# Kernel tuning notes

Measured on AMD Instinct MI355X. Metric: run time of the kernel, lower is better.

Reference implementation:

```python
import jax, jax.numpy as jnp
import numpy as np

B, T, D = 16, 4096, 512
N_SLOTS = 64


def setup_inputs() -> dict:
    key = jax.random.key(0)
    ks = jax.random.split(key, 7)
    s = 1.0 / np.sqrt(D)  # keep tanh out of deep saturation, like orthogonal*0.9 init
    return {
        "x_seq": jax.random.normal(ks[0], (B, T, D), jnp.float32),
        "h_tape": jax.random.normal(ks[1], (B, N_SLOTS, D), jnp.float32) * 0.1,
        "h_work": jax.random.normal(ks[2], (B, D), jnp.float32) * 0.1,
        "W_h": jax.random.normal(ks[3], (D, D), jnp.float32) * s,
        "W_x": jax.random.normal(ks[4], (D, D), jnp.float32) * s,
        "b_h": jnp.zeros((D,), jnp.float32),
        "W_write": jax.random.normal(ks[5], (D, D), jnp.float32) * s,
    }


def reference(x_seq, h_tape, h_work, W_h, W_x, b_h, W_write):
    """Dual-memory Elman recurrence.

    Per step t:
      read_t  = softmax(h_tape @ h_work / sqrt(D)) @ h_tape   (content-based tape read)
      h_work  = tanh(W_h h_work + W_x x_t + read_t + b_h)
      tape write: slot (t mod n_slots) <- W_write h_work      (FIFO tape write)
    Returns (h_work_out [B,T,D], h_tape_final [B,S,D], last h_work [B,D]).
    """
    scale = jnp.asarray(1.0 / np.sqrt(D), x_seq.dtype)

    def step(carry, inp):
        tape, h = carry
        x_t, t = inp
        scores = jnp.einsum("bsd,bd->bs", tape, h) * scale        # [B,S]
        attn = jax.nn.softmax(scores, axis=-1)
        read = jnp.einsum("bs,bsd->bd", attn, tape)               # [B,D]
        h_new = jnp.tanh(h @ W_h.T + x_t @ W_x.T + read + b_h)    # [B,D]
        w_vec = h_new @ W_write.T                                 # [B,D]
        slot = t % N_SLOTS
        tape = jax.lax.dynamic_update_slice(tape, w_vec[:, None, :], (0, slot, 0))
        return (tape, h_new), h_new

    xs = (jnp.swapaxes(x_seq, 0, 1), jnp.arange(x_seq.shape[1]))
    (tape_f, _), h_seq = jax.lax.scan(step, (h_tape, h_work), xs)
    h_work_out = jnp.swapaxes(h_seq, 0, 1)  # [B,T,D]
    return h_work_out, tape_f, h_work_out[:, -1]
```

## Files before the change

### kernel.cpp

```cpp
#include <hip/hip_runtime.h>
#include <cstddef>

#define B_SZ   16
#define T_SZ   4096
#define D_SZ   512
#define NSLOT  64
#define NW     16
#define RPW    32
#define TP     36
#define SCALE  0.044194173824159216f

__device__ __align__(8) unsigned long long g_ps2[B_SZ * NW * NSLOT];
__device__ __align__(8) unsigned long long g_hx2[B_SZ * D_SZ];

#define AL(p)    __hip_atomic_load((p),  __ATOMIC_RELAXED, __HIP_MEMORY_SCOPE_AGENT)
#define AS(p,v)  __hip_atomic_store((p), (v), __ATOMIC_RELAXED, __HIP_MEMORY_SCOPE_AGENT)

__device__ __forceinline__ unsigned long long pk(float v, unsigned tag) {
    return ((unsigned long long)tag << 32) | (unsigned long long)__float_as_uint(v);
}

__global__ __launch_bounds__(256)
void xw_gemm_kernel(const float* __restrict__ X, const float* __restrict__ Wx,
                    const float* __restrict__ bh, float* __restrict__ out)
{
    __shared__ float As[16][68];
    __shared__ float Bs[16][68];
    const int m0 = blockIdx.x * 64;
    const int n0 = blockIdx.y * 64;
    const int tid = threadIdx.x;
    const int tr = tid >> 4, tc = tid & 15;
    const int lrow = tid >> 2;
    const int lkk  = (tid & 3) * 4;

    float acc[4][4] = {};

    for (int k0 = 0; k0 < D_SZ; k0 += 16) {
        float4 av = *(const float4*)(X  + (size_t)(m0 + lrow) * D_SZ + k0 + lkk);
        float4 bv = *(const float4*)(Wx + (size_t)(n0 + lrow) * D_SZ + k0 + lkk);
        As[lkk+0][lrow] = av.x; As[lkk+1][lrow] = av.y;
        As[lkk+2][lrow] = av.z; As[lkk+3][lrow] = av.w;
        Bs[lkk+0][lrow] = bv.x; Bs[lkk+1][lrow] = bv.y;
        Bs[lkk+2][lrow] = bv.z; Bs[lkk+3][lrow] = bv.w;
        __syncthreads();
        #pragma unroll
        for (int kk = 0; kk < 16; ++kk) {
            float a[4], b[4];
            #pragma unroll
            for (int i = 0; i < 4; ++i) a[i] = As[kk][tr*4+i];
            #pragma unroll
            for (int j = 0; j < 4; ++j) b[j] = Bs[kk][tc*4+j];
            #pragma unroll
            for (int i = 0; i < 4; ++i)
                #pragma unroll
                for (int j = 0; j < 4; ++j)
                    acc[i][j] = fmaf(a[i], b[j], acc[i][j]);
        }
        __syncthreads();
    }
    #pragma unroll
    for (int i = 0; i < 4; ++i) {
        const int m = m0 + tr*4 + i;
        const int n = n0 + tc*4;
        float4 o;
        o.x = acc[i][0] + bh[n+0];
        o.y = acc[i][1] + bh[n+1];
        o.z = acc[i][2] + bh[n+2];
        o.w = acc[i][3] + bh[n+3];
        *(float4*)(out + (size_t)m * D_SZ + n) = o;
    }
}

__global__ __launch_bounds__(256, 1)
void recurrence_mw(const float* __restrict__ tape0, const float* __restrict__ h0,
                   const float* __restrict__ W_h, const float* __restrict__ W_w,
                   float* __restrict__ out)
{
    __shared__ float tp[NSLOT][TP];
    __shared__ float hh[D_SZ];
    __shared__ float ps_l[NSLOT];
    __shared__ float attn[NSLOT];
    __shared__ float zmv[RPW];
    __shared__ float rp8[8][RPW];

    const int blk = blockIdx.x;
    const int xcd = blk & 7;
    const int jj0 = blk >> 3;
    const int b   = xcd * 2 + (jj0 & 1);
    const int w   = jj0 >> 1;
    const int R0  = w * RPW;
    const int tid = threadIdx.x;
    const int fb  = b * NW;
    const int g16 = tid >> 4, sj = tid & 15;

    if (tid < NSLOT) AS(&g_ps2[(size_t)(fb + w) * NSLOT + tid], 0ULL);
    if (tid < RPW)   AS(&g_hx2[(size_t)b * D_SZ + R0 + tid], 0ULL);

    float4 wh0[8], wh1[8], ww0[8], ww1[8];
    {
        const float* a0 = W_h + (size_t)(R0 + g16)      * D_SZ + 4 * sj;
        const float* a1 = W_h + (size_t)(R0 + g16 + 16) * D_SZ + 4 * sj;
        const float* b0 = W_w + (size_t)(R0 + g16)      * D_SZ + 4 * sj;
        const float* b1 = W_w + (size_t)(R0 + g16 + 16) * D_SZ + 4 * sj;
        #pragma unroll
        for (int i = 0; i < 8; ++i) {
            wh0[i] = *(const float4*)(a0 + 64 * i);
            wh1[i] = *(const float4*)(a1 + 64 * i);
            ww0[i] = *(const float4*)(b0 + 64 * i);
            ww1[i] = *(const float4*)(b1 + 64 * i);
        }
    }

    for (int i = tid; i < NSLOT * RPW; i += 256) {
        const int s = i >> 5, jc = i & 31;
        tp[s][jc] = tape0[((size_t)b * NSLOT + s) * D_SZ + R0 + jc];
    }
    for (int i = tid; i < D_SZ; i += 256) hh[i] = h0[(size_t)b * D_SZ + i];
    __syncthreads();

    float* outb = out + (size_t)b * T_SZ * D_SZ;

    const int sA = tid >> 2, qA = tid & 3;
    const int jB = tid & 31, sg = tid >> 5;

    for (int t = 0; t < T_SZ; ++t) {
        const unsigned tg = (unsigned)(t + 1);
        float xwv = 0.f;
        if (tid < RPW) xwv = outb[(size_t)t * D_SZ + R0 + tid];

        {
            float4 t0 = *(const float4*)&tp[sA][qA * 8];
            float4 t1 = *(const float4*)&tp[sA][qA * 8 + 4];
            float4 ha = *(const float4*)&hh[R0 + qA * 8];
            float4 hb = *(const float4*)&hh[R0 + qA * 8 + 4];
            float acc = t0.x*ha.x + t0.y*ha.y + t0.z*ha.z + t0.w*ha.w
                      + t1.x*hb.x + t1.y*hb.y + t1.z*hb.z + t1.w*hb.w;
            acc += __shfl_xor(acc, 1);
            acc += __shfl_xor(acc, 2);
            if (qA == 0) ps_l[sA] = acc;
        }
        __syncthreads();

        if (tid < NSLOT)
            AS(&g_ps2[(size_t)(fb + w) * NSLOT + tid], pk(ps_l[tid], tg));

        {
            float a0 = 0.f, a1 = 0.f;
            #pragma unroll
            for (int i = 0; i < 8; ++i) {
                float4 hr = *(const float4*)&hh[4 * sj + 64 * i];
                a0 = fmaf(wh0[i].x, hr.x, a0);
                a0 = fmaf(wh0[i].y, hr.y, a0);
                a0 = fmaf(wh0[i].z, hr.z, a0);
                a0 = fmaf(wh0[i].w, hr.w, a0);
                a1 = fmaf(wh1[i].x, hr.x, a1);
                a1 = fmaf(wh1[i].y, hr.y, a1);
                a1 = fmaf(wh1[i].z, hr.z, a1);
                a1 = fmaf(wh1[i].w, hr.w, a1);
            }
            a0 += __shfl_xor(a0, 1); a1 += __shfl_xor(a1, 1);
            a0 += __shfl_xor(a0, 2); a1 += __shfl_xor(a1, 2);
            a0 += __shfl_xor(a0, 4); a1 += __shfl_xor(a1, 4);
            a0 += __shfl_xor(a0, 8); a1 += __shfl_xor(a1, 8);
            if (sj == 0) { zmv[g16] = a0; zmv[g16 + 16] = a1; }
        }

        {
            const unsigned long long* pp = &g_ps2[(size_t)(fb + qA * 4) * NSLOT + sA];
            unsigned long long v0, v1, v2, v3;
            for (;;) {
                v0 = AL(pp + 0 * NSLOT); v1 = AL(pp + 1 * NSLOT);
                v2 = AL(pp + 2 * NSLOT); v3 = AL(pp + 3 * NSLOT);
                if ((unsigned)(v0 >> 32) == tg && (unsigned)(v1 >> 32) == tg &&
                    (unsigned)(v2 >> 32) == tg && (unsigned)(v3 >> 32) == tg) break;
                __builtin_amdgcn_s_sleep(1);
            }
            float acc = __uint_as_float((unsigned)v0) + __uint_as_float((unsigned)v1)
                      + __uint_as_float((unsigned)v2) + __uint_as_float((unsigned)v3);
            acc += __shfl_xor(acc, 1);
            acc += __shfl_xor(acc, 2);
            if (qA == 0) ps_l[sA] = acc * SCALE;
        }
        __syncthreads();

        if (tid < 64) {
            const float v = ps_l[tid];
            float m = v;
            #pragma unroll
            for (int o = 32; o; o >>= 1) m = fmaxf(m, __shfl_xor(m, o));
            const float e = __expf(v - m);
            float s = e;
            #pragma unroll
            for (int o = 32; o; o >>= 1) s += __shfl_xor(s, o);
            attn[tid] = e / s;
        }
        __syncthreads();

        {
            float acc = 0.f;
            #pragma unroll
            for (int s8 = 0; s8 < 8; ++s8)
                acc = fmaf(attn[sg * 8 + s8], tp[sg * 8 + s8][jB], acc);
            rp8[sg][jB] = acc;
        }
        __syncthreads();

        if (tid < RPW) {
            const float rr = rp8[0][tid] + rp8[1][tid] + rp8[2][tid] + rp8[3][tid]
                           + rp8[4][tid] + rp8[5][tid] + rp8[6][tid] + rp8[7][tid];
            const float v = tanhf(zmv[tid] + rr + xwv);
            outb[(size_t)t * D_SZ + R0 + tid] = v;
            AS(&g_hx2[(size_t)b * D_SZ + R0 + tid], pk(v, tg));
        }

        {
            const int d0 = tid * 2;
            const unsigned long long* hp = &g_hx2[(size_t)b * D_SZ + d0];
            unsigned long long v0, v1;
            for (;;) {
                v0 = AL(hp); v1 = AL(hp + 1);
                if ((unsigned)(v0 >> 32) == tg && (unsigned)(v1 >> 32) == tg) break;
                __builtin_amdgcn_s_sleep(1);
            }
            hh[d0]     = __uint_as_float((unsigned)v0);
            hh[d0 + 1] = __uint_as_float((unsigned)v1);
        }
        __syncthreads();

        {
            const int slot = t & (NSLOT - 1);
            float a0 = 0.f, a1 = 0.f;
            #pragma unroll
            for (int i = 0; i < 8; ++i) {
                float4 hr = *(const float4*)&hh[4 * sj + 64 * i];
                a0 = fmaf(ww0[i].x, hr.x, a0);
                a0 = fmaf(ww0[i].y, hr.y, a0);
                a0 = fmaf(ww0[i].z, hr.z, a0);
                a0 = fmaf(ww0[i].w, hr.w, a0);
                a1 = fmaf(ww1[i].x, hr.x, a1);
                a1 = fmaf(ww1[i].y, hr.y, a1);
                a1 = fmaf(ww1[i].z, hr.z, a1);
                a1 = fmaf(ww1[i].w, hr.w, a1);
            }
            a0 += __shfl_xor(a0, 1); a1 += __shfl_xor(a1, 1);
            a0 += __shfl_xor(a0, 2); a1 += __shfl_xor(a1, 2);
            a0 += __shfl_xor(a0, 4); a1 += __shfl_xor(a1, 4);
            a0 += __shfl_xor(a0, 8); a1 += __shfl_xor(a1, 8);
            if (sj == 0) {
                tp[slot][g16]      = a0;
                tp[slot][g16 + 16] = a1;
            }
        }
        __syncthreads();
    }

    float* tout = out + (size_t)B_SZ * T_SZ * D_SZ + (size_t)b * NSLOT * D_SZ;
    for (int i = tid; i < NSLOT * RPW; i += 256) {
        const int s = i >> 5, jc = i & 31;
        tout[(size_t)s * D_SZ + R0 + jc] = tp[s][jc];
    }
    if (tid < RPW) {
        float* lout = out + (size_t)B_SZ * T_SZ * D_SZ
                          + (size_t)B_SZ * NSLOT * D_SZ + (size_t)b * D_SZ;
        lout[R0 + tid] = hh[R0 + tid];
    }
}

extern "C" void kernel_launch(void* const* d_in, const int* in_sizes, int n_in,
                              void* d_out, int out_size, void* d_ws, size_t ws_size,
                              hipStream_t stream)
{
    const float* x_seq   = (const float*)d_in[0];
    const float* h_tape  = (const float*)d_in[1];
    const float* h_work  = (const float*)d_in[2];
    const float* W_h     = (const float*)d_in[3];
    const float* W_x     = (const float*)d_in[4];
    const float* b_h     = (const float*)d_in[5];
    const float* W_write = (const float*)d_in[6];
    float* out = (float*)d_out;

    dim3 g1(T_SZ * B_SZ / 64, D_SZ / 64);
    xw_gemm_kernel<<<g1, 256, 0, stream>>>(x_seq, W_x, b_h, out);

    recurrence_mw<<<B_SZ * NW, 256, 0, stream>>>(h_tape, h_work, W_h, W_write, out);
}
```

Baseline: 15.92 ms.

## Defer tape write to next step and merge per-step grid syncs into one

The per-step schedule is restructured. Each step now does a single combined spin-wait for the partial attention scores and the new h, where before there were two separate cross-block waits. The W_write matvec is folded into the same pass as the W_h matvec on the next step. The newly written slot's score is handled by a small extra exchange (g_q) and a softmax correction, which takes the write off the critical path between h publication and the next step's scores. In exchange it adds a per-step wait on the single-slot dot product, extra softmax bookkeeping, and a final-step flush, which raises correctness risk.

```diff
diff --git a/kernel.cpp b/kernel.cpp
--- a/kernel.cpp
+++ b/kernel.cpp
@@ -10,14 +10,18 @@
 #define TP     36
 #define SCALE  0.044194173824159216f
 
-__device__ __align__(8) unsigned long long g_ps2[B_SZ * NW * NSLOT];
-__device__ __align__(8) unsigned long long g_hx2[B_SZ * D_SZ];
+__device__ __align__(8) unsigned long long g_pb[B_SZ * NW * NSLOT];
+__device__ __align__(8) unsigned long long g_hb[B_SZ * D_SZ];
+__device__ __align__(8) unsigned long long g_q [B_SZ * NW];
 
 #define AL(p)    __hip_atomic_load((p),  __ATOMIC_RELAXED, __HIP_MEMORY_SCOPE_AGENT)
 #define AS(p,v)  __hip_atomic_store((p), (v), __ATOMIC_RELAXED, __HIP_MEMORY_SCOPE_AGENT)
 
 __device__ __forceinline__ unsigned long long pk(float v, unsigned tag) {
     return ((unsigned long long)tag << 32) | (unsigned long long)__float_as_uint(v);
+}
+__device__ __forceinline__ float lo(unsigned long long v) {
+    return __uint_as_float((unsigned)v);
 }
 
 __global__ __launch_bounds__(256)
@@ -76,12 +80,14 @@
                    const float* __restrict__ W_h, const float* __restrict__ W_w,
                    float* __restrict__ out)
 {
-    __shared__ float tp[NSLOT][TP];
-    __shared__ float hh[D_SZ];
-    __shared__ float ps_l[NSLOT];
-    __shared__ float attn[NSLOT];
+    __shared__ __align__(16) float tp[NSLOT][TP];
+    __shared__ __align__(16) float hh[D_SZ];
+    __shared__ __align__(16) float hno[RPW];
+    __shared__ float scr[NSLOT];
+    __shared__ float es[NSLOT];
     __shared__ float zmv[RPW];
     __shared__ float rp8[8][RPW];
+    __shared__ float sml[2];
 
     const int blk = blockIdx.x;
     const int xcd = blk & 7;
@@ -92,9 +98,12 @@
     const int tid = threadIdx.x;
     const int fb  = b * NW;
     const int g16 = tid >> 4, sj = tid & 15;
-
-    if (tid < NSLOT) AS(&g_ps2[(size_t)(fb + w) * NSLOT + tid], 0ULL);
-    if (tid < RPW)   AS(&g_hx2[(size_t)b * D_SZ + R0 + tid], 0ULL);
+    const int sA  = tid >> 2, qA = tid & 3;
+    const int sg  = tid >> 5, jB = tid & 31;
+
+    if (tid < NSLOT) AS(&g_pb[((size_t)fb + w) * NSLOT + tid], 0ULL);
+    if (tid < RPW)   AS(&g_hb[(size_t)b * D_SZ + R0 + tid], 0ULL);
+    if (tid == 0)    AS(&g_q[fb + w], 0ULL);
 
     float4 wh0[8], wh1[8], ww0[8], ww1[8];
     {
@@ -112,79 +121,88 @@
     }
 
     for (int i = tid; i < NSLOT * RPW; i += 256) {
-        const int s = i >> 5, jc = i & 31;
-        tp[s][jc] = tape0[((size_t)b * NSLOT + s) * D_SZ + R0 + jc];
+        const int s = i >> 5, j = i & 31;
+        tp[s][j] = tape0[((size_t)b * NSLOT + s) * D_SZ + R0 + j];
     }
     for (int i = tid; i < D_SZ; i += 256) hh[i] = h0[(size_t)b * D_SZ + i];
     __syncthreads();
 
     float* outb = out + (size_t)b * T_SZ * D_SZ;
 
-    const int sA = tid >> 2, qA = tid & 3;
-    const int jB = tid & 31, sg = tid >> 5;
+    if (tid < RPW) {
+        hno[tid] = hh[R0 + tid];
+        AS(&g_hb[(size_t)b * D_SZ + R0 + tid], pk(hh[R0 + tid], 1u));
+    }
+    __syncthreads();
+    {
+        const float* trow = &tp[sA][8 * qA];
+        float4 t0 = *(const float4*)trow;
+        float4 t1 = *(const float4*)(trow + 4);
+        float4 h0v = *(const float4*)&hno[8 * qA];
+        float4 h1v = *(const float4*)&hno[8 * qA + 4];
+        float pp = t0.x*h0v.x + t0.y*h0v.y + t0.z*h0v.z + t0.w*h0v.w
+                 + t1.x*h1v.x + t1.y*h1v.y + t1.z*h1v.z + t1.w*h1v.w;
+        pp += __shfl_xor(pp, 1);
+        pp += __shfl_xor(pp, 2);
+        if (qA == 0) AS(&g_pb[((size_t)fb + w) * NSLOT + sA], pk(pp, 1u));
+    }
 
     for (int t = 0; t < T_SZ; ++t) {
-        const unsigned tg = (unsigned)(t + 1);
+        const unsigned tgB = (unsigned)(t + 1);
+        const int sp = (t - 1) & 63;
+
         float xwv = 0.f;
         if (tid < RPW) xwv = outb[(size_t)t * D_SZ + R0 + tid];
-
         {
-            float4 t0 = *(const float4*)&tp[sA][qA * 8];
-            float4 t1 = *(const float4*)&tp[sA][qA * 8 + 4];
-            float4 ha = *(const float4*)&hh[R0 + qA * 8];
-            float4 hb = *(const float4*)&hh[R0 + qA * 8 + 4];
-            float acc = t0.x*ha.x + t0.y*ha.y + t0.z*ha.z + t0.w*ha.w
-                      + t1.x*hb.x + t1.y*hb.y + t1.z*hb.z + t1.w*hb.w;
-            acc += __shfl_xor(acc, 1);
-            acc += __shfl_xor(acc, 2);
-            if (qA == 0) ps_l[sA] = acc;
-        }
-        __syncthreads();
-
-        if (tid < NSLOT)
-            AS(&g_ps2[(size_t)(fb + w) * NSLOT + tid], pk(ps_l[tid], tg));
+            const unsigned long long* pb = &g_pb[((size_t)fb + qA * 4) * NSLOT + sA];
+            const unsigned long long* hb = &g_hb[(size_t)b * D_SZ + 2 * tid];
+            unsigned long long p0, p1, p2, p3, v0, v1;
+            for (;;) {
+                p0 = AL(pb);              p1 = AL(pb + NSLOT);
+                p2 = AL(pb + 2 * NSLOT);  p3 = AL(pb + 3 * NSLOT);
+                v0 = AL(hb);              v1 = AL(hb + 1);
+                if ((unsigned)(p0 >> 32) == tgB && (unsigned)(p1 >> 32) == tgB &&
+                    (unsigned)(p2 >> 32) == tgB && (unsigned)(p3 >> 32) == tgB &&
+                    (unsigned)(v0 >> 32) == tgB && (unsigned)(v1 >> 32) == tgB) break;
+                __builtin_amdgcn_s_sleep(1);
+            }
+            float s4 = lo(p0) + lo(p1) + lo(p2) + lo(p3);
+            s4 += __shfl_xor(s4, 1);
+            s4 += __shfl_xor(s4, 2);
+            if (qA == 0) scr[sA] = s4 * SCALE;
+            hh[2 * tid]     = lo(v0);
+            hh[2 * tid + 1] = lo(v1);
+        }
+        __syncthreads();
 
         {
-            float a0 = 0.f, a1 = 0.f;
+            float z0 = 0.f, z1 = 0.f, v0 = 0.f, v1 = 0.f;
             #pragma unroll
             for (int i = 0; i < 8; ++i) {
                 float4 hr = *(const float4*)&hh[4 * sj + 64 * i];
-                a0 = fmaf(wh0[i].x, hr.x, a0);
-                a0 = fmaf(wh0[i].y, hr.y, a0);
-                a0 = fmaf(wh0[i].z, hr.z, a0);
-                a0 = fmaf(wh0[i].w, hr.w, a0);
-                a1 = fmaf(wh1[i].x, hr.x, a1);
-                a1 = fmaf(wh1[i].y, hr.y, a1);
-                a1 = fmaf(wh1[i].z, hr.z, a1);
-                a1 = fmaf(wh1[i].w, hr.w, a1);
-            }
-            a0 += __shfl_xor(a0, 1); a1 += __shfl_xor(a1, 1);
-            a0 += __shfl_xor(a0, 2); a1 += __shfl_xor(a1, 2);
-            a0 += __shfl_xor(a0, 4); a1 += __shfl_xor(a1, 4);
-            a0 += __shfl_xor(a0, 8); a1 += __shfl_xor(a1, 8);
-            if (sj == 0) { zmv[g16] = a0; zmv[g16 + 16] = a1; }
-        }
-
-        {
-            const unsigned long long* pp = &g_ps2[(size_t)(fb + qA * 4) * NSLOT + sA];
-            unsigned long long v0, v1, v2, v3;
-            for (;;) {
-                v0 = AL(pp + 0 * NSLOT); v1 = AL(pp + 1 * NSLOT);
-                v2 = AL(pp + 2 * NSLOT); v3 = AL(pp + 3 * NSLOT);
-                if ((unsigned)(v0 >> 32) == tg && (unsigned)(v1 >> 32) == tg &&
-                    (unsigned)(v2 >> 32) == tg && (unsigned)(v3 >> 32) == tg) break;
-                __builtin_amdgcn_s_sleep(1);
-            }
-            float acc = __uint_as_float((unsigned)v0) + __uint_as_float((unsigned)v1)
-                      + __uint_as_float((unsigned)v2) + __uint_as_float((unsigned)v3);
-            acc += __shfl_xor(acc, 1);
-            acc += __shfl_xor(acc, 2);
-            if (qA == 0) ps_l[sA] = acc * SCALE;
+                z0 = fmaf(wh0[i].x, hr.x, z0); z0 = fmaf(wh0[i].y, hr.y, z0);
+                z0 = fmaf(wh0[i].z, hr.z, z0); z0 = fmaf(wh0[i].w, hr.w, z0);
+                z1 = fmaf(wh1[i].x, hr.x, z1); z1 = fmaf(wh1[i].y, hr.y, z1);
+                z1 = fmaf(wh1[i].z, hr.z, z1); z1 = fmaf(wh1[i].w, hr.w, z1);
+                v0 = fmaf(ww0[i].x, hr.x, v0); v0 = fmaf(ww0[i].y, hr.y, v0);
+                v0 = fmaf(ww0[i].z, hr.z, v0); v0 = fmaf(ww0[i].w, hr.w, v0);
+                v1 = fmaf(ww1[i].x, hr.x, v1); v1 = fmaf(ww1[i].y, hr.y, v1);
+                v1 = fmaf(ww1[i].z, hr.z, v1); v1 = fmaf(ww1[i].w, hr.w, v1);
+            }
+            #pragma unroll
+            for (int o = 1; o <= 8; o <<= 1) {
+                z0 += __shfl_xor(z0, o); z1 += __shfl_xor(z1, o);
+                v0 += __shfl_xor(v0, o); v1 += __shfl_xor(v1, o);
+            }
+            if (sj == 0) {
+                zmv[g16] = z0; zmv[g16 + 16] = z1;
+                if (t > 0) { tp[sp][g16] = v0; tp[sp][g16 + 16] = v1; }
+            }
         }
         __syncthreads();
 
         if (tid < 64) {
-            const float v = ps_l[tid];
+            const float v = (t > 0 && tid == sp) ? -3.0e38f : scr[tid];
             float m = v;
             #pragma unroll
             for (int o = 32; o; o >>= 1) m = fmaxf(m, __shfl_xor(m, o));
@@ -192,7 +210,14 @@
             float s = e;
             #pragma unroll
             for (int o = 32; o; o >>= 1) s += __shfl_xor(s, o);
-            attn[tid] = e / s;
+            es[tid] = e;
+            if (tid == 0) { sml[0] = m; sml[1] = s; }
+        } else if (tid < 96 && t > 0) {
+            const int ld = tid - 64;
+            float qp = tp[sp][ld] * hh[R0 + ld];
+            #pragma unroll
+            for (int o = 1; o <= 16; o <<= 1) qp += __shfl_xor(qp, o);
+            if (ld == 0) AS(&g_q[fb + w], pk(qp, tgB));
         }
         __syncthreads();
 
@@ -200,7 +225,7 @@
             float acc = 0.f;
             #pragma unroll
             for (int s8 = 0; s8 < 8; ++s8)
-                acc = fmaf(attn[sg * 8 + s8], tp[sg * 8 + s8][jB], acc);
+                acc = fmaf(es[sg * 8 + s8], tp[sg * 8 + s8][jB], acc);
             rp8[sg][jB] = acc;
         }
         __syncthreads();
@@ -208,61 +233,81 @@
         if (tid < RPW) {
             const float rr = rp8[0][tid] + rp8[1][tid] + rp8[2][tid] + rp8[3][tid]
                            + rp8[4][tid] + rp8[5][tid] + rp8[6][tid] + rp8[7][tid];
-            const float v = tanhf(zmv[tid] + rr + xwv);
-            outb[(size_t)t * D_SZ + R0 + tid] = v;
-            AS(&g_hx2[(size_t)b * D_SZ + R0 + tid], pk(v, tg));
-        }
+            float rd;
+            if (t > 0) {
+                const unsigned long long* qp_ = &g_q[fb + (tid & 15)];
+                unsigned long long qv;
+                for (;;) {
+                    qv = AL(qp_);
+                    if ((unsigned)(qv >> 32) == tgB) break;
+                    __builtin_amdgcn_s_sleep(1);
+                }
+                float qs = lo(qv);
+                qs += __shfl_xor(qs, 1); qs += __shfl_xor(qs, 2);
+                qs += __shfl_xor(qs, 4); qs += __shfl_xor(qs, 8);
+                const float esig = __expf(qs * SCALE - sml[0]);
+                rd = (rr + esig * tp[sp][tid]) / (sml[1] + esig);
+            } else {
+                rd = rr / sml[1];
+            }
+            const float hn = tanhf(zmv[tid] + rd + xwv);
+            outb[(size_t)t * D_SZ + R0 + tid] = hn;
+            AS(&g_hb[(size_t)b * D_SZ + R0 + tid], pk(hn, (unsigned)(t + 2)));
+            hno[tid] = hn;
+        }
+        __syncthreads();
 
         {
-            const int d0 = tid * 2;
-            const unsigned long long* hp = &g_hx2[(size_t)b * D_SZ + d0];
-            unsigned long long v0, v1;
-            for (;;) {
-                v0 = AL(hp); v1 = AL(hp + 1);
-                if ((unsigned)(v0 >> 32) == tg && (unsigned)(v1 >> 32) == tg) break;
-                __builtin_amdgcn_s_sleep(1);
-            }
-            hh[d0]     = __uint_as_float((unsigned)v0);
-            hh[d0 + 1] = __uint_as_float((unsigned)v1);
-        }
-        __syncthreads();
-
-        {
-            const int slot = t & (NSLOT - 1);
-            float a0 = 0.f, a1 = 0.f;
-            #pragma unroll
-            for (int i = 0; i < 8; ++i) {
-                float4 hr = *(const float4*)&hh[4 * sj + 64 * i];
-                a0 = fmaf(ww0[i].x, hr.x, a0);
-                a0 = fmaf(ww0[i].y, hr.y, a0);
-                a0 = fmaf(ww0[i].z, hr.z, a0);
-                a0 = fmaf(ww0[i].w, hr.w, a0);
-                a1 = fmaf(ww1[i].x, hr.x, a1);
-                a1 = fmaf(ww1[i].y, hr.y, a1);
-                a1 = fmaf(ww1[i].z, hr.z, a1);
-                a1 = fmaf(ww1[i].w, hr.w, a1);
-            }
-            a0 += __shfl_xor(a0, 1); a1 += __shfl_xor(a1, 1);
-            a0 += __shfl_xor(a0, 2); a1 += __shfl_xor(a1, 2);
-            a0 += __shfl_xor(a0, 4); a1 += __shfl_xor(a1, 4);
-            a0 += __shfl_xor(a0, 8); a1 += __shfl_xor(a1, 8);
-            if (sj == 0) {
-                tp[slot][g16]      = a0;
-                tp[slot][g16 + 16] = a1;
-            }
-        }
-        __syncthreads();
-    }
-
+            const float* trow = &tp[sA][8 * qA];
+            float4 t0 = *(const float4*)trow;
+            float4 t1 = *(const float4*)(trow + 4);
+            float4 h0v = *(const float4*)&hno[8 * qA];
+            float4 h1v = *(const float4*)&hno[8 * qA + 4];
+            float pp = t0.x*h0v.x + t0.y*h0v.y + t0.z*h0v.z + t0.w*h0v.w
+                     + t1.x*h1v.x + t1.y*h1v.y + t1.z*h1v.z + t1.w*h1v.w;
+            pp += __shfl_xor(pp, 1);
+            pp += __shfl_xor(pp, 2);
+            if (qA == 0) AS(&g_pb[((size_t)fb + w) * NSLOT + sA], pk(pp, (unsigned)(t + 2)));
+        }
+    }
+
+    {
+        const unsigned long long* hb = &g_hb[(size_t)b * D_SZ + 2 * tid];
+        unsigned long long v0, v1;
+        const unsigned tgF = (unsigned)(T_SZ + 1);
+        for (;;) {
+            v0 = AL(hb); v1 = AL(hb + 1);
+            if ((unsigned)(v0 >> 32) == tgF && (unsigned)(v1 >> 32) == tgF) break;
+            __builtin_amdgcn_s_sleep(1);
+        }
+        hh[2 * tid]     = lo(v0);
+        hh[2 * tid + 1] = lo(v1);
+    }
+    __syncthreads();
+    {
+        float v0 = 0.f, v1 = 0.f;
+        #pragma unroll
+        for (int i = 0; i < 8; ++i) {
+            float4 hr = *(const float4*)&hh[4 * sj + 64 * i];
+            v0 = fmaf(ww0[i].x, hr.x, v0); v0 = fmaf(ww0[i].y, hr.y, v0);
+            v0 = fmaf(ww0[i].z, hr.z, v0); v0 = fmaf(ww0[i].w, hr.w, v0);
+            v1 = fmaf(ww1[i].x, hr.x, v1); v1 = fmaf(ww1[i].y, hr.y, v1);
+            v1 = fmaf(ww1[i].z, hr.z, v1); v1 = fmaf(ww1[i].w, hr.w, v1);
+        }
+        #pragma unroll
+        for (int o = 1; o <= 8; o <<= 1) { v0 += __shfl_xor(v0, o); v1 += __shfl_xor(v1, o); }
+        if (sj == 0) { tp[63][g16] = v0; tp[63][g16 + 16] = v1; }
+    }
+    __syncthreads();
     float* tout = out + (size_t)B_SZ * T_SZ * D_SZ + (size_t)b * NSLOT * D_SZ;
     for (int i = tid; i < NSLOT * RPW; i += 256) {
-        const int s = i >> 5, jc = i & 31;
-        tout[(size_t)s * D_SZ + R0 + jc] = tp[s][jc];
-    }
-    if (tid < RPW) {
+        const int s = i >> 5, j = i & 31;
+        tout[(size_t)s * D_SZ + R0 + j] = tp[s][j];
+    }
+    if (w == 0) {
         float* lout = out + (size_t)B_SZ * T_SZ * D_SZ
                           + (size_t)B_SZ * NSLOT * D_SZ + (size_t)b * D_SZ;
-        lout[R0 + tid] = hh[R0 + tid];
+        for (int i = tid; i < D_SZ; i += 256) lout[i] = hh[i];
     }
 }
 
```

After: 18.40 ms. +15.6%, slower.
